# Kernel optimization log

Measured on AMD Instinct MI355X. Metric: run time of the kernel, lower is better.

Reference implementation:

```python
import jax, jax.numpy as jnp
import numpy as np

V, E, H, B, S = 32000, 512, 1024, 128, 512
NEG = -1e9


def setup_inputs() -> dict:
    key = jax.random.key(0)
    ks = jax.random.split(key, 12)
    s = 0.02
    return {
        "previous_word": jax.random.randint(ks[0], (B, 1), 0, V),
        "h_0": jax.random.normal(ks[1], (B, H), jnp.float32),
        "c_0": jax.random.normal(ks[2], (B, H), jnp.float32),
        "ctx": jax.random.normal(ks[3], (B, S, H), jnp.float32),
        "ctx_mask": jnp.zeros((B, S), dtype=bool),
        "emb": jax.random.normal(ks[4], (V, E), jnp.float32) * s,
        "W_ih": jax.random.normal(ks[5], (4 * H, E), jnp.float32) * s,
        "W_hh": jax.random.normal(ks[6], (4 * H, H), jnp.float32) * s,
        "b_ih": jnp.zeros((4 * H,), jnp.float32),
        "b_hh": jnp.zeros((4 * H,), jnp.float32),
        "W_in": jax.random.normal(ks[7], (H, H), jnp.float32) * s,
        "W_out": jax.random.normal(ks[8], (H, 2 * H), jnp.float32) * s,
        "W_dec": jax.random.normal(ks[9], (V, H), jnp.float32) * s,
        "b_dec": jnp.zeros((V,), jnp.float32),
    }


def reference(previous_word, h_0, c_0, ctx, ctx_mask, emb, W_ih, W_hh, b_ih, b_hh, W_in, W_out, W_dec, b_dec):
    # embedding lookup + squeeze; dropout is identity in eval mode
    x = emb[previous_word[:, 0]]                       # [B, E]
    # LSTMCell: gate order i, f, g, o (PyTorch convention)
    gates = x @ W_ih.T + b_ih + h_0 @ W_hh.T + b_hh    # [B, 4H]
    i, f, g, o = jnp.split(gates, 4, axis=1)
    i = jax.nn.sigmoid(i)
    f = jax.nn.sigmoid(f)
    g = jnp.tanh(g)
    o = jax.nn.sigmoid(o)
    c_1 = f * c_0 + i * g
    h_1 = o * jnp.tanh(c_1)
    # SoftDotAttention
    target = h_1 @ W_in.T                               # [B, H]
    attn = jnp.einsum('bsh,bh->bs', ctx, target)        # [B, S]
    attn = jnp.where(ctx_mask, NEG, attn)
    alpha = jax.nn.softmax(attn, axis=1)
    weighted = jnp.einsum('bs,bsh->bh', alpha, ctx)     # [B, H]
    h_tilde = jnp.tanh(jnp.concatenate([weighted, h_1], axis=1) @ W_out.T)
    logit = h_tilde @ W_dec.T + b_dec                   # [B, V]
    return (h_1, c_1, alpha, logit)
```

## Files before the change

### kernel.cpp

```cpp
#include <hip/hip_runtime.h>
#include <hip/hip_bf16.h>
#include <cstdint>

#define NEG_BIG (-1.0e9f)

typedef __attribute__((ext_vector_type(8))) short short8_t;
typedef __attribute__((ext_vector_type(4))) float f32x4;

typedef __attribute__((address_space(1))) const unsigned int gu32_t;
typedef __attribute__((address_space(3))) unsigned int lu32_t;

__device__ __forceinline__ short f2bf(float x) {
  union { float f; unsigned u; } v; v.f = x;
  unsigned r = v.u + 0x7fffu + ((v.u >> 16) & 1u);
  return (short)(r >> 16);
}
__device__ __forceinline__ float sigmoidf_(float x) { return 1.0f / (1.0f + __expf(-x)); }

__device__ __forceinline__ void lds_barrier() {
  asm volatile("s_waitcnt lgkmcnt(0)\n\ts_barrier" ::: "memory");
}
__device__ __forceinline__ void block_barrier() {
  asm volatile("" ::: "memory");
  __builtin_amdgcn_s_barrier();
  asm volatile("" ::: "memory");
}

__launch_bounds__(256, 2)
__global__ void k_gates(const int* __restrict__ prev, const float* __restrict__ emb,
                        const float* __restrict__ h0,
                        const float* __restrict__ W_ih, const float* __restrict__ W_hh,
                        const float* __restrict__ b_ih, const float* __restrict__ b_hh,
                        const float* __restrict__ c0,
                        float* __restrict__ h1_out, float* __restrict__ c1_out,
                        short* __restrict__ A3) {
  __shared__ __align__(16) short lA[2][64 * 64];
  __shared__ __align__(16) short lW[2][64 * 64];
  const int tid = threadIdx.x;
  const int wid = tid >> 6, l = tid & 63, l15 = l & 15, khalf = l >> 4;
  const int hb = blockIdx.x;
  const int mrow0 = blockIdx.y * 64;

  const int arow = tid >> 2;
  const int apart = tid & 3;
  const int aswz = (arow & 7) << 4;
  const int bA = mrow0 + arow;
  const int pv = prev[bA];
  const float* embrow = emb + (size_t)pv * 512 + apart * 16;
  const float* h0row = h0 + (size_t)bA * 1024 + apart * 16;

  int wrow_[4], wkq_[4];
  const float* wih_[4];
  const float* whh_[4];
#pragma unroll
  for (int j = 0; j < 4; ++j) {
    int idx = j * 1024 + tid * 4;
    int n = idx >> 6;
    wkq_[j] = idx & 63;
    wrow_[j] = n;
    int grow = (n >> 4) * 1024 + hb * 16 + (n & 15);
    wih_[j] = W_ih + (size_t)grow * 512;
    whh_[j] = W_hh + (size_t)grow * 1024;
  }

  f32x4 acc[4];
#pragma unroll
  for (int r = 0; r < 4; ++r) acc[r] = (f32x4){0.f, 0.f, 0.f, 0.f};

  float4 aF[4], wR[4];
  auto stage_regs = [&](int k0) {
    const float* asrc = (k0 < 512) ? (embrow + k0) : (h0row + (k0 - 512));
#pragma unroll
    for (int q = 0; q < 4; ++q) aF[q] = *(const float4*)(asrc + q * 4);
#pragma unroll
    for (int j = 0; j < 4; ++j) {
      int kg = k0 + wkq_[j];
      wR[j] = (kg < 512) ? *(const float4*)(wih_[j] + kg)
                         : *(const float4*)(whh_[j] + (kg - 512));
    }
  };
  auto write_lds = [&](int buf) {
    char* drow = (char*)lA[buf] + arow * 128;
#pragma unroll
    for (int q = 0; q < 2; ++q) {
      short8_t s;
      s[0] = f2bf(aF[2 * q].x); s[1] = f2bf(aF[2 * q].y);
      s[2] = f2bf(aF[2 * q].z); s[3] = f2bf(aF[2 * q].w);
      s[4] = f2bf(aF[2 * q + 1].x); s[5] = f2bf(aF[2 * q + 1].y);
      s[6] = f2bf(aF[2 * q + 1].z); s[7] = f2bf(aF[2 * q + 1].w);
      *(short8_t*)(drow + ((apart * 32 + q * 16) ^ aswz)) = s;
    }
#pragma unroll
    for (int j = 0; j < 4; ++j) {
      short4 h4;
      h4.x = f2bf(wR[j].x); h4.y = f2bf(wR[j].y); h4.z = f2bf(wR[j].z); h4.w = f2bf(wR[j].w);
      *(short4*)((char*)lW[buf] + wrow_[j] * 128 + ((wkq_[j] * 2) ^ ((wrow_[j] & 7) << 4))) = h4;
    }
  };
  auto compute = [&](int buf) {
#pragma unroll
    for (int ks = 0; ks < 2; ++ks) {
      const int ubyte = ks * 64 + khalf * 16;
      const int nrow = wid * 16 + l15;
      short8_t bfrag = *(const short8_t*)((char*)lW[buf] + nrow * 128 + (ubyte ^ ((nrow & 7) << 4)));
#pragma unroll
      for (int r = 0; r < 4; ++r) {
        const int mrow = r * 16 + l15;
        short8_t afrag = *(const short8_t*)((char*)lA[buf] + mrow * 128 + (ubyte ^ ((mrow & 7) << 4)));
        acc[r] = __builtin_amdgcn_mfma_f32_16x16x32_bf16(afrag, bfrag, acc[r], 0, 0, 0);
      }
    }
  };

  stage_regs(0);
  write_lds(0);
  for (int t = 0; t < 24; ++t) {
    const int cur = t & 1;
    if (t + 1 < 24) stage_regs((t + 1) << 6);
    lds_barrier();
    compute(cur);
    if (t + 1 < 24) write_lds(cur ^ 1);
  }

  lds_barrier();
  float* gbuf = (float*)&lA[0][0];
#pragma unroll
  for (int r = 0; r < 4; ++r)
#pragma unroll
    for (int e = 0; e < 4; ++e)
      gbuf[wid * 1024 + (r * 16 + khalf * 4 + e) * 16 + l15] = acc[r][e];
  __syncthreads();
#pragma unroll
  for (int q = 0; q < 4; ++q) {
    int idx = q * 256 + tid;
    int hloc = idx & 15, mloc = idx >> 4;
    int b = mrow0 + mloc;
    int hh = hb * 16 + hloc;
    float iv = gbuf[0 + mloc * 16 + hloc] + b_ih[hh] + b_hh[hh];
    float fv = gbuf[1024 + mloc * 16 + hloc] + b_ih[1024 + hh] + b_hh[1024 + hh];
    float gv = gbuf[2048 + mloc * 16 + hloc] + b_ih[2048 + hh] + b_hh[2048 + hh];
    float ov = gbuf[3072 + mloc * 16 + hloc] + b_ih[3072 + hh] + b_hh[3072 + hh];
    float c1 = sigmoidf_(fv) * c0[(size_t)b * 1024 + hh] + sigmoidf_(iv) * tanhf(gv);
    float h1 = sigmoidf_(ov) * tanhf(c1);
    c1_out[(size_t)b * 1024 + hh] = c1;
    h1_out[(size_t)b * 1024 + hh] = h1;
    A3[(size_t)b * 2048 + 1024 + hh] = f2bf(h1);
  }
}

template <int MB, int WN, int EPI>
__launch_bounds__(256, 2)
__global__ void k_gemm(const short* __restrict__ A, int lda,
                       const float* __restrict__ Wa, int ldwa, int Ka,
                       const float* __restrict__ Wb, int ldwb, int Ktot,
                       const float* __restrict__ bias0, const float* __restrict__ bias1,
                       float* __restrict__ outF, short* __restrict__ outB, int ldo) {
  constexpr int BN = WN * 16;
  constexpr int MREP = (MB == 128) ? 2 * WN : 1;
  constexpr int AU = MB / 32;
  constexpr int WLOADS = (BN * 64) / 1024;
  __shared__ __align__(16) short lA[2][MB * 64];
  __shared__ __align__(16) short lW[2][BN * 64];
  const int tid = threadIdx.x;
  const int wid = tid >> 6, l = tid & 63, l15 = l & 15, khalf = l >> 4;
  const int nblk = blockIdx.x;
  const int mrow0 = blockIdx.y * MB;
  const int m_wave = (WN == 1) ? wid * (MB / 4) : 0;
  const int nb_local = (WN == 4) ? wid * 16 : 0;

  const int arow = (MB == 128) ? (tid >> 1) : (tid >> 2);
  const int apart = (MB == 128) ? (tid & 1) : (tid & 3);
  const int abase = apart * (AU * 16);
  const int aswz = (arow & 7) << 4;
  const short* Arow = A + (size_t)(mrow0 + arow) * lda + apart * (AU * 8);

  int wn_[WLOADS], wkq_[WLOADS];
#pragma unroll
  for (int j = 0; j < WLOADS; ++j) {
    int idx = j * 1024 + tid * 4;
    wn_[j] = idx >> 6;
    wkq_[j] = idx & 63;
  }

  f32x4 acc[MREP];
#pragma unroll
  for (int r = 0; r < MREP; ++r) acc[r] = (f32x4){0.f, 0.f, 0.f, 0.f};

  short8_t aR[AU];
  float4 wR[WLOADS];

  auto stage_regs = [&](int k0) {
#pragma unroll
    for (int q = 0; q < AU; ++q) aR[q] = *(const short8_t*)(Arow + k0 + q * 8);
#pragma unroll
    for (int j = 0; j < WLOADS; ++j) {
      int kg = k0 + wkq_[j];
      const float* p = (kg < Ka) ? (Wa + (size_t)(nblk * BN + wn_[j]) * ldwa + kg)
                                 : (Wb + (size_t)(nblk * BN + wn_[j]) * ldwb + (kg - Ka));
      wR[j] = *(const float4*)p;
    }
  };
  auto write_lds = [&](int buf) {
    char* drow = (char*)lA[buf] + arow * 128;
#pragma unroll
    for (int q = 0; q < AU; ++q)
      *(short8_t*)(drow + ((abase + q * 16) ^ aswz)) = aR[q];
#pragma unroll
    for (int j = 0; j < WLOADS; ++j) {
      short4 h4;
      h4.x = f2bf(wR[j].x); h4.y = f2bf(wR[j].y); h4.z = f2bf(wR[j].z); h4.w = f2bf(wR[j].w);
      *(short4*)((char*)lW[buf] + wn_[j] * 128 + ((wkq_[j] * 2) ^ ((wn_[j] & 7) << 4))) = h4;
    }
  };
  auto compute = [&](int buf) {
#pragma unroll
    for (int ks = 0; ks < 2; ++ks) {
      const int ubyte = ks * 64 + khalf * 16;
      const int nrow = nb_local + l15;
      short8_t bfrag = *(const short8_t*)((char*)lW[buf] + nrow * 128 + (ubyte ^ ((nrow & 7) << 4)));
#pragma unroll
      for (int r = 0; r < MREP; ++r) {
        const int mrow = m_wave + r * 16 + l15;
        short8_t afrag = *(const short8_t*)((char*)lA[buf] + mrow * 128 + (ubyte ^ ((mrow & 7) << 4)));
        acc[r] = __builtin_amdgcn_mfma_f32_16x16x32_bf16(afrag, bfrag, acc[r], 0, 0, 0);
      }
    }
  };

  const int NT = Ktot >> 6;
  stage_regs(0);
  write_lds(0);
  for (int t = 0; t < NT; ++t) {
    const int cur = t & 1;
    if (t + 1 < NT) stage_regs((t + 1) << 6);
    lds_barrier();
    compute(cur);
    if (t + 1 < NT) write_lds(cur ^ 1);
  }

  const int n = nblk * BN + nb_local + l15;
  float bias = 0.f;
  if (bias0) bias = bias0[n];
  if (bias1) bias += bias1[n];
#pragma unroll
  for (int r = 0; r < MREP; ++r) {
    int mb = mrow0 + m_wave + r * 16 + khalf * 4;
#pragma unroll
    for (int e = 0; e < 4; ++e) {
      float v = acc[r][e] + bias;
      if (EPI == 1) {
        outB[(size_t)(mb + e) * ldo + n] = f2bf(tanhf(v));
      } else {
        outF[(size_t)(mb + e) * ldo + n] = v;
      }
    }
  }
}

__launch_bounds__(256, 2)
__global__ void k_attn(const float* __restrict__ ctx, const float* __restrict__ target,
                       const unsigned char* __restrict__ mask,
                       float* __restrict__ scores, float* __restrict__ part) {
  __shared__ __align__(16) float lds[2][8 * 1024];
  const int b = blockIdx.x >> 2, chunk = blockIdx.x & 3;
  const int tid = threadIdx.x;
  const int wid = tid >> 6, l = tid & 63;
  const float* tg = target + (size_t)b * 1024;
  float4 t4[4], w4[4];
#pragma unroll
  for (int j = 0; j < 4; ++j) {
    t4[j] = *(const float4*)(tg + j * 256 + l * 4);
    w4[j].x = 0.f; w4[j].y = 0.f; w4[j].z = 0.f; w4[j].w = 0.f;
  }
  float m = -INFINITY, lsum = 0.f;
  const int s0 = chunk * 128;
  const float* cb = ctx + ((size_t)b * 512 + s0) * 1024;
  const unsigned char* mk = mask + (size_t)b * 512 + s0;

  auto stage = [&](int buf, int tt) {
    const char* src = (const char*)(cb + (size_t)tt * 8192);
    char* dst = (char*)&lds[buf][0];
#pragma unroll
    for (int i = 0; i < 8; ++i) {
      const int off = i * 4096 + tid * 16;
      __builtin_amdgcn_global_load_lds((gu32_t*)(src + off), (lu32_t*)(dst + off), 16, 0, 0);
    }
  };

  stage(0, 0);
  int buf = 0;
  for (int t = 0; t < 16; ++t) {
    if (t < 15) {
      stage(buf ^ 1, t + 1);
      asm volatile("s_waitcnt vmcnt(8)" ::: "memory");
    } else {
      asm volatile("s_waitcnt vmcnt(0)" ::: "memory");
    }
    block_barrier();
#pragma unroll
    for (int rr = 0; rr < 2; ++rr) {
      const int r = wid * 2 + rr;
      const float* row = &lds[buf][r * 1024];
      float4 c0 = *(const float4*)(row + l * 4);
      float4 c1 = *(const float4*)(row + 256 + l * 4);
      float4 c2 = *(const float4*)(row + 512 + l * 4);
      float4 c3 = *(const float4*)(row + 768 + l * 4);
      float p = c0.x * t4[0].x + c0.y * t4[0].y + c0.z * t4[0].z + c0.w * t4[0].w +
                c1.x * t4[1].x + c1.y * t4[1].y + c1.z * t4[1].z + c1.w * t4[1].w +
                c2.x * t4[2].x + c2.y * t4[2].y + c2.z * t4[2].z + c2.w * t4[2].w +
                c3.x * t4[3].x + c3.y * t4[3].y + c3.z * t4[3].z + c3.w * t4[3].w;
#pragma unroll
      for (int off = 32; off > 0; off >>= 1) p += __shfl_xor(p, off);
      const int sg = t * 8 + r;
      if (mk[sg]) p = NEG_BIG;
      if (l == 0) scores[(size_t)b * 512 + s0 + sg] = p;
      float mn = fmaxf(m, p);
      float scale = __expf(m - mn);
      float e = __expf(p - mn);
      lsum = lsum * scale + e;
      w4[0].x = w4[0].x * scale + e * c0.x; w4[0].y = w4[0].y * scale + e * c0.y;
      w4[0].z = w4[0].z * scale + e * c0.z; w4[0].w = w4[0].w * scale + e * c0.w;
      w4[1].x = w4[1].x * scale + e * c1.x; w4[1].y = w4[1].y * scale + e * c1.y;
      w4[1].z = w4[1].z * scale + e * c1.z; w4[1].w = w4[1].w * scale + e * c1.w;
      w4[2].x = w4[2].x * scale + e * c2.x; w4[2].y = w4[2].y * scale + e * c2.y;
      w4[2].z = w4[2].z * scale + e * c2.z; w4[2].w = w4[2].w * scale + e * c2.w;
      w4[3].x = w4[3].x * scale + e * c3.x; w4[3].y = w4[3].y * scale + e * c3.y;
      w4[3].z = w4[3].z * scale + e * c3.z; w4[3].w = w4[3].w * scale + e * c3.w;
      m = mn;
    }
    block_barrier();
    buf ^= 1;
  }
  float* pp = part + ((size_t)b * 16 + (chunk * 4 + wid)) * 1028;
#pragma unroll
  for (int j = 0; j < 4; ++j) *(float4*)(pp + j * 256 + l * 4) = w4[j];
  if (l == 0) { pp[1024] = m; pp[1025] = lsum; }
}

__launch_bounds__(256, 4)
__global__ void k_finish(const float* __restrict__ scores, const float* __restrict__ part,
                         float* __restrict__ alpha, short* __restrict__ A3) {
  __shared__ float sm[16], sl[16];
  int b = blockIdx.x, t = threadIdx.x;
  if (t < 16) {
    sm[t] = part[((size_t)b * 16 + t) * 1028 + 1024];
    sl[t] = part[((size_t)b * 16 + t) * 1028 + 1025];
  }
  __syncthreads();
  float M = -INFINITY;
#pragma unroll
  for (int i = 0; i < 16; ++i) M = fmaxf(M, sm[i]);
  float scl[16];
  float L = 0.f;
#pragma unroll
  for (int i = 0; i < 16; ++i) {
    scl[i] = __expf(sm[i] - M);
    L += sl[i] * scl[i];
  }
  float inv = 1.0f / L;
  float s0 = scores[(size_t)b * 512 + t];
  float s1 = scores[(size_t)b * 512 + 256 + t];
  alpha[(size_t)b * 512 + t] = __expf(s0 - M) * inv;
  alpha[(size_t)b * 512 + 256 + t] = __expf(s1 - M) * inv;
  float ax = 0.f, ay = 0.f, az = 0.f, aw = 0.f;
#pragma unroll
  for (int i = 0; i < 16; ++i) {
    const float4 w = *(const float4*)(part + ((size_t)b * 16 + i) * 1028 + t * 4);
    ax += scl[i] * w.x; ay += scl[i] * w.y; az += scl[i] * w.z; aw += scl[i] * w.w;
  }
  short4 o4;
  o4.x = f2bf(ax * inv); o4.y = f2bf(ay * inv); o4.z = f2bf(az * inv); o4.w = f2bf(aw * inv);
  *(short4*)(A3 + (size_t)b * 2048 + t * 4) = o4;
}

extern "C" void kernel_launch(void* const* d_in, const int* in_sizes, int n_in,
                              void* d_out, int out_size, void* d_ws, size_t ws_size,
                              hipStream_t stream) {
  const int* prev = (const int*)d_in[0];
  const float* h0 = (const float*)d_in[1];
  const float* c0 = (const float*)d_in[2];
  const float* ctx = (const float*)d_in[3];
  const unsigned char* mask = (const unsigned char*)d_in[4];
  const float* emb = (const float*)d_in[5];
  const float* W_ih = (const float*)d_in[6];
  const float* W_hh = (const float*)d_in[7];
  const float* b_ih = (const float*)d_in[8];
  const float* b_hh = (const float*)d_in[9];
  const float* W_in = (const float*)d_in[10];
  const float* W_out = (const float*)d_in[11];
  const float* W_dec = (const float*)d_in[12];
  const float* b_dec = (const float*)d_in[13];

  float* out_h1 = (float*)d_out;
  float* out_c1 = out_h1 + 128 * 1024;
  float* out_alpha = out_c1 + 128 * 1024;
  float* out_logit = out_alpha + 128 * 512;

  char* ws = (char*)d_ws;
  short* A3 = (short*)(ws + 0x000000);
  float* target = (float*)(ws + 0x100000);
  float* scores = (float*)(ws + 0x200000);
  float* part = (float*)(ws + 0x300000);
  short* htilde = (short*)(ws + 0xD00000);

  k_gates<<<dim3(64, 2), 256, 0, stream>>>(prev, emb, h0, W_ih, W_hh, b_ih, b_hh, c0,
                                           out_h1, out_c1, A3);
  k_gemm<64, 1, 0><<<dim3(64, 2), 256, 0, stream>>>(A3 + 1024, 2048, W_in, 1024, 1024, W_in,
                                                    1024, 1024, nullptr, nullptr, target,
                                                    nullptr, 1024);
  k_attn<<<512, 256, 0, stream>>>(ctx, target, mask, scores, part);
  k_finish<<<128, 256, 0, stream>>>(scores, part, out_alpha, A3);
  k_gemm<64, 1, 1><<<dim3(64, 2), 256, 0, stream>>>(A3, 2048, W_out, 2048, 2048, W_out, 2048,
                                                    2048, nullptr, nullptr, nullptr, htilde,
                                                    1024);
  k_gemm<128, 4, 0><<<dim3(500, 1), 256, 0, stream>>>(htilde, 1024, W_dec, 1024, 1024, W_dec,
                                                      1024, 1024, b_dec, nullptr, out_logit,
                                                      nullptr, 32000);
}
```

Measured before the change: 149.2 us.

## Split-K small GEMMs and fuse attention combine into W_out GEMM

The W_in projection now runs as a 4-way split-K GEMM over all 128 rows, and its partial sums are added up inside the attention kernel. Attention blocks merge their four waves' online-softmax partials in LDS before writing, so only four partials per batch row go to memory. The separate finish kernel is removed: a new split-K W_out GEMM builds the normalized context rows on the fly from those partials. A small kernel then reduces the 8 K-slices, applies tanh, and writes alpha. The aim is more parallelism on the latency-bound small GEMMs and fewer serial launches, at the cost of extra partial-sum traffic and repeated softmax-coefficient math.

```diff
diff --git a/kernel.cpp b/kernel.cpp
--- a/kernel.cpp
+++ b/kernel.cpp
@@ -154,13 +154,18 @@
                        const float* __restrict__ Wa, int ldwa, int Ka,
                        const float* __restrict__ Wb, int ldwb, int Ktot,
                        const float* __restrict__ bias0, const float* __restrict__ bias1,
-                       float* __restrict__ outF, short* __restrict__ outB, int ldo) {
+                       float* __restrict__ outF, short* __restrict__ outB, int ldo,
+                       int kstride, size_t pstride) {
   constexpr int BN = WN * 16;
   constexpr int MREP = (MB == 128) ? 2 * WN : 1;
   constexpr int AU = MB / 32;
   constexpr int WLOADS = (BN * 64) / 1024;
   __shared__ __align__(16) short lA[2][MB * 64];
   __shared__ __align__(16) short lW[2][BN * 64];
+  const int kc = blockIdx.z;
+  A += (size_t)kc * kstride;
+  Wa += (size_t)kc * kstride;
+  if (outF) outF += (size_t)kc * pstride;
   const int tid = threadIdx.x;
   const int wid = tid >> 6, l = tid & 63, l15 = l & 15, khalf = l >> 4;
   const int nblk = blockIdx.x;
@@ -258,18 +263,24 @@
 }
 
 __launch_bounds__(256, 2)
-__global__ void k_attn(const float* __restrict__ ctx, const float* __restrict__ target,
+__global__ void k_attn(const float* __restrict__ ctx, const float* __restrict__ tp,
                        const unsigned char* __restrict__ mask,
                        float* __restrict__ scores, float* __restrict__ part) {
   __shared__ __align__(16) float lds[2][8 * 1024];
+  __shared__ float sml[8];
   const int b = blockIdx.x >> 2, chunk = blockIdx.x & 3;
   const int tid = threadIdx.x;
   const int wid = tid >> 6, l = tid & 63;
-  const float* tg = target + (size_t)b * 1024;
   float4 t4[4], w4[4];
 #pragma unroll
   for (int j = 0; j < 4; ++j) {
-    t4[j] = *(const float4*)(tg + j * 256 + l * 4);
+    float4 a = {0.f, 0.f, 0.f, 0.f};
+#pragma unroll
+    for (int p = 0; p < 4; ++p) {
+      const float4 v = *(const float4*)(tp + (size_t)p * 131072 + (size_t)b * 1024 + j * 256 + l * 4);
+      a.x += v.x; a.y += v.y; a.z += v.z; a.w += v.w;
+    }
+    t4[j] = a;
     w4[j].x = 0.f; w4[j].y = 0.f; w4[j].z = 0.f; w4[j].w = 0.f;
   }
   float m = -INFINITY, lsum = 0.f;
@@ -331,46 +342,162 @@
     block_barrier();
     buf ^= 1;
   }
-  float* pp = part + ((size_t)b * 16 + (chunk * 4 + wid)) * 1028;
-#pragma unroll
-  for (int j = 0; j < 4; ++j) *(float4*)(pp + j * 256 + l * 4) = w4[j];
-  if (l == 0) { pp[1024] = m; pp[1025] = lsum; }
-}
-
-__launch_bounds__(256, 4)
-__global__ void k_finish(const float* __restrict__ scores, const float* __restrict__ part,
-                         float* __restrict__ alpha, short* __restrict__ A3) {
-  __shared__ float sm[16], sl[16];
-  int b = blockIdx.x, t = threadIdx.x;
-  if (t < 16) {
-    sm[t] = part[((size_t)b * 16 + t) * 1028 + 1024];
-    sl[t] = part[((size_t)b * 16 + t) * 1028 + 1025];
-  }
+
+  float* cbuf = &lds[0][0];
+#pragma unroll
+  for (int j = 0; j < 4; ++j) *(float4*)(cbuf + wid * 1024 + j * 256 + l * 4) = w4[j];
+  if (l == 0) { sml[wid] = m; sml[4 + wid] = lsum; }
   __syncthreads();
-  float M = -INFINITY;
-#pragma unroll
-  for (int i = 0; i < 16; ++i) M = fmaxf(M, sm[i]);
-  float scl[16];
-  float L = 0.f;
-#pragma unroll
-  for (int i = 0; i < 16; ++i) {
-    scl[i] = __expf(sm[i] - M);
-    L += sl[i] * scl[i];
-  }
-  float inv = 1.0f / L;
-  float s0 = scores[(size_t)b * 512 + t];
-  float s1 = scores[(size_t)b * 512 + 256 + t];
-  alpha[(size_t)b * 512 + t] = __expf(s0 - M) * inv;
-  alpha[(size_t)b * 512 + 256 + t] = __expf(s1 - M) * inv;
-  float ax = 0.f, ay = 0.f, az = 0.f, aw = 0.f;
-#pragma unroll
-  for (int i = 0; i < 16; ++i) {
-    const float4 w = *(const float4*)(part + ((size_t)b * 16 + i) * 1028 + t * 4);
-    ax += scl[i] * w.x; ay += scl[i] * w.y; az += scl[i] * w.z; aw += scl[i] * w.w;
-  }
-  short4 o4;
-  o4.x = f2bf(ax * inv); o4.y = f2bf(ay * inv); o4.z = f2bf(az * inv); o4.w = f2bf(aw * inv);
-  *(short4*)(A3 + (size_t)b * 2048 + t * 4) = o4;
+  const float M = fmaxf(fmaxf(sml[0], sml[1]), fmaxf(sml[2], sml[3]));
+  const float sc0 = __expf(sml[0] - M), sc1 = __expf(sml[1] - M);
+  const float sc2 = __expf(sml[2] - M), sc3 = __expf(sml[3] - M);
+  const float L = sml[4] * sc0 + sml[5] * sc1 + sml[6] * sc2 + sml[7] * sc3;
+  const float4 v0 = *(const float4*)(cbuf + 0 * 1024 + tid * 4);
+  const float4 v1 = *(const float4*)(cbuf + 1 * 1024 + tid * 4);
+  const float4 v2 = *(const float4*)(cbuf + 2 * 1024 + tid * 4);
+  const float4 v3 = *(const float4*)(cbuf + 3 * 1024 + tid * 4);
+  float4 o;
+  o.x = v0.x * sc0 + v1.x * sc1 + v2.x * sc2 + v3.x * sc3;
+  o.y = v0.y * sc0 + v1.y * sc1 + v2.y * sc2 + v3.y * sc3;
+  o.z = v0.z * sc0 + v1.z * sc1 + v2.z * sc2 + v3.z * sc3;
+  o.w = v0.w * sc0 + v1.w * sc1 + v2.w * sc2 + v3.w * sc3;
+  float* pp = part + ((size_t)b * 4 + chunk) * 1028;
+  *(float4*)(pp + tid * 4) = o;
+  if (tid == 0) { pp[1024] = M; pp[1025] = L; }
+}
+
+__launch_bounds__(256, 2)
+__global__ void k_wgemm(const short* __restrict__ A3, const float* __restrict__ part,
+                        const float* __restrict__ W_out, float* __restrict__ wp) {
+  __shared__ __align__(16) short lA[2][128 * 64];
+  __shared__ __align__(16) short lW[2][16 * 64];
+  const int kc = blockIdx.z, nblk = blockIdx.x;
+  const int tid = threadIdx.x;
+  const int wid = tid >> 6, l = tid & 63, l15 = l & 15, khalf = l >> 4;
+  const int arow = tid >> 1, apart = tid & 1;
+  const int aswz = (arow & 7) << 4;
+  const bool wpath = (kc < 4);
+
+  const int colbase = kc * 256 + apart * 32;
+  const short* ArowB = A3 + (size_t)arow * 2048 + colbase;
+  const float* ps = part + (size_t)arow * 4 * 1028;
+  const float* pr0 = ps + colbase;
+  const float* pr1 = ps + 1028 + colbase;
+  const float* pr2 = ps + 2056 + colbase;
+  const float* pr3 = ps + 3084 + colbase;
+  float coef0 = 0.f, coef1 = 0.f, coef2 = 0.f, coef3 = 0.f;
+  if (wpath) {
+    float m0 = ps[1024], l0 = ps[1025], m1 = ps[1028 + 1024], l1 = ps[1028 + 1025];
+    float m2 = ps[2056 + 1024], l2 = ps[2056 + 1025], m3 = ps[3084 + 1024], l3 = ps[3084 + 1025];
+    float M = fmaxf(fmaxf(m0, m1), fmaxf(m2, m3));
+    float s0 = __expf(m0 - M), s1 = __expf(m1 - M), s2 = __expf(m2 - M), s3 = __expf(m3 - M);
+    float inv = 1.0f / (l0 * s0 + l1 * s1 + l2 * s2 + l3 * s3);
+    coef0 = s0 * inv; coef1 = s1 * inv; coef2 = s2 * inv; coef3 = s3 * inv;
+  }
+
+  const int wn = (tid * 4) >> 6, wkq = (tid * 4) & 63;
+  const float* wrow = W_out + (size_t)(nblk * 16 + wn) * 2048 + kc * 256;
+
+  f32x4 acc[2];
+  acc[0] = (f32x4){0.f, 0.f, 0.f, 0.f};
+  acc[1] = (f32x4){0.f, 0.f, 0.f, 0.f};
+  float4 aC[8];
+  short8_t aB[4];
+  float4 wR;
+
+  auto stage_regs = [&](int k0) {
+    if (wpath) {
+#pragma unroll
+      for (int q = 0; q < 8; ++q) {
+        const float4 v0 = *(const float4*)(pr0 + k0 + q * 4);
+        const float4 v1 = *(const float4*)(pr1 + k0 + q * 4);
+        const float4 v2 = *(const float4*)(pr2 + k0 + q * 4);
+        const float4 v3 = *(const float4*)(pr3 + k0 + q * 4);
+        aC[q].x = coef0 * v0.x + coef1 * v1.x + coef2 * v2.x + coef3 * v3.x;
+        aC[q].y = coef0 * v0.y + coef1 * v1.y + coef2 * v2.y + coef3 * v3.y;
+        aC[q].z = coef0 * v0.z + coef1 * v1.z + coef2 * v2.z + coef3 * v3.z;
+        aC[q].w = coef0 * v0.w + coef1 * v1.w + coef2 * v2.w + coef3 * v3.w;
+      }
+    } else {
+#pragma unroll
+      for (int q = 0; q < 4; ++q) aB[q] = *(const short8_t*)(ArowB + k0 + q * 8);
+    }
+    wR = *(const float4*)(wrow + k0 + wkq);
+  };
+  auto write_lds = [&](int buf) {
+    char* drow = (char*)lA[buf] + arow * 128;
+    if (wpath) {
+#pragma unroll
+      for (int q2 = 0; q2 < 4; ++q2) {
+        short8_t s;
+        s[0] = f2bf(aC[2 * q2].x); s[1] = f2bf(aC[2 * q2].y);
+        s[2] = f2bf(aC[2 * q2].z); s[3] = f2bf(aC[2 * q2].w);
+        s[4] = f2bf(aC[2 * q2 + 1].x); s[5] = f2bf(aC[2 * q2 + 1].y);
+        s[6] = f2bf(aC[2 * q2 + 1].z); s[7] = f2bf(aC[2 * q2 + 1].w);
+        *(short8_t*)(drow + ((apart * 64 + q2 * 16) ^ aswz)) = s;
+      }
+    } else {
+#pragma unroll
+      for (int q = 0; q < 4; ++q)
+        *(short8_t*)(drow + ((apart * 64 + q * 16) ^ aswz)) = aB[q];
+    }
+    short4 h4;
+    h4.x = f2bf(wR.x); h4.y = f2bf(wR.y); h4.z = f2bf(wR.z); h4.w = f2bf(wR.w);
+    *(short4*)((char*)lW[buf] + wn * 128 + ((wkq * 2) ^ ((wn & 7) << 4))) = h4;
+  };
+  auto compute = [&](int buf) {
+#pragma unroll
+    for (int ks = 0; ks < 2; ++ks) {
+      const int ubyte = ks * 64 + khalf * 16;
+      short8_t bfrag = *(const short8_t*)((char*)lW[buf] + l15 * 128 + (ubyte ^ ((l15 & 7) << 4)));
+#pragma unroll
+      for (int r = 0; r < 2; ++r) {
+        const int mrow = wid * 32 + r * 16 + l15;
+        short8_t afrag = *(const short8_t*)((char*)lA[buf] + mrow * 128 + (ubyte ^ ((mrow & 7) << 4)));
+        acc[r] = __builtin_amdgcn_mfma_f32_16x16x32_bf16(afrag, bfrag, acc[r], 0, 0, 0);
+      }
+    }
+  };
+
+  stage_regs(0);
+  write_lds(0);
+  for (int t = 0; t < 4; ++t) {
+    const int cur = t & 1;
+    if (t + 1 < 4) stage_regs((t + 1) << 6);
+    lds_barrier();
+    compute(cur);
+    if (t + 1 < 4) write_lds(cur ^ 1);
+  }
+
+  const int n = nblk * 16 + l15;
+  float* out = wp + (size_t)kc * 131072;
+#pragma unroll
+  for (int r = 0; r < 2; ++r) {
+    int mb = wid * 32 + r * 16 + khalf * 4;
+#pragma unroll
+    for (int e = 0; e < 4; ++e)
+      out[(size_t)(mb + e) * 1024 + n] = acc[r][e];
+  }
+}
+
+__global__ void k_fin2(const float* __restrict__ wp, const float* __restrict__ part,
+                       const float* __restrict__ scores, short* __restrict__ ht,
+                       float* __restrict__ alpha) {
+  int t = blockIdx.x * 256 + threadIdx.x;
+  float s = 0.f;
+#pragma unroll
+  for (int p = 0; p < 8; ++p) s += wp[(size_t)p * 131072 + t];
+  ht[t] = f2bf(tanhf(s));
+  if (t < 65536) {
+    int b = t >> 9, si = t & 511;
+    const float* ps = part + (size_t)b * 4 * 1028;
+    float m0 = ps[1024], l0 = ps[1025], m1 = ps[1028 + 1024], l1 = ps[1028 + 1025];
+    float m2 = ps[2056 + 1024], l2 = ps[2056 + 1025], m3 = ps[3084 + 1024], l3 = ps[3084 + 1025];
+    float M = fmaxf(fmaxf(m0, m1), fmaxf(m2, m3));
+    float L = l0 * __expf(m0 - M) + l1 * __expf(m1 - M) + l2 * __expf(m2 - M) +
+              l3 * __expf(m3 - M);
+    alpha[t] = __expf(scores[(size_t)b * 512 + si] - M) / L;
+  }
 }
 
 extern "C" void kernel_launch(void* const* d_in, const int* in_sizes, int n_in,
@@ -398,22 +525,21 @@
 
   char* ws = (char*)d_ws;
   short* A3 = (short*)(ws + 0x000000);
-  float* target = (float*)(ws + 0x100000);
-  float* scores = (float*)(ws + 0x200000);
-  float* part = (float*)(ws + 0x300000);
-  short* htilde = (short*)(ws + 0xD00000);
+  float* scores = (float*)(ws + 0x100000);
+  float* tp = (float*)(ws + 0x200000);
+  float* part = (float*)(ws + 0x400000);
+  float* wp = (float*)(ws + 0x700000);
+  short* htilde = (short*)(ws + 0xB00000);
 
   k_gates<<<dim3(64, 2), 256, 0, stream>>>(prev, emb, h0, W_ih, W_hh, b_ih, b_hh, c0,
                                            out_h1, out_c1, A3);
-  k_gemm<64, 1, 0><<<dim3(64, 2), 256, 0, stream>>>(A3 + 1024, 2048, W_in, 1024, 1024, W_in,
-                                                    1024, 1024, nullptr, nullptr, target,
-                                                    nullptr, 1024);
-  k_attn<<<512, 256, 0, stream>>>(ctx, target, mask, scores, part);
-  k_finish<<<128, 256, 0, stream>>>(scores, part, out_alpha, A3);
-  k_gemm<64, 1, 1><<<dim3(64, 2), 256, 0, stream>>>(A3, 2048, W_out, 2048, 2048, W_out, 2048,
-                                                    2048, nullptr, nullptr, nullptr, htilde,
-                                                    1024);
-  k_gemm<128, 4, 0><<<dim3(500, 1), 256, 0, stream>>>(htilde, 1024, W_dec, 1024, 1024, W_dec,
-                                                      1024, 1024, b_dec, nullptr, out_logit,
-                                                      nullptr, 32000);
-}
+  k_gemm<128, 1, 0><<<dim3(64, 1, 4), 256, 0, stream>>>(
+      A3 + 1024, 2048, W_in, 1024, 1 << 30, W_in, 1024, 256, nullptr, nullptr, tp, nullptr,
+      1024, 256, (size_t)131072);
+  k_attn<<<512, 256, 0, stream>>>(ctx, tp, mask, scores, part);
+  k_wgemm<<<dim3(64, 1, 8), 256, 0, stream>>>(A3, part, W_out, wp);
+  k_fin2<<<512, 256, 0, stream>>>(wp, part, scores, htilde, out_alpha);
+  k_gemm<128, 4, 0><<<dim3(500, 1, 1), 256, 0, stream>>>(
+      htilde, 1024, W_dec, 1024, 1024, W_dec, 1024, 1024, b_dec, nullptr, out_logit, nullptr,
+      32000, 0, 0);
+}
```

After: 144.1 us. 3.4% less time.
